# Performance work log

Hardware: AMD Instinct MI355X
Metric: run time of the kernel (lower is better)

The kernel has to match this reference:

```python
import jax, jax.numpy as jnp
import numpy as np
import math

HEADS = 8

def setup_inputs() -> dict:
    key = jax.random.key(0)
    k1, k2 = jax.random.split(key)
    B, C, H, W = 8, 512, 32, 32
    x = jax.random.normal(k1, (B, C, H, W), dtype=jnp.float32)
    # weight-norm 1x1 conv params: v ~ N(0, 0.05), g initialized to ||v|| (torch weight_norm default)
    proj_v = jax.random.normal(k2, (3 * C, C), dtype=jnp.float32) * 0.05
    proj_g = jnp.linalg.norm(proj_v, axis=1)
    proj_b = jnp.zeros((3 * C,), dtype=jnp.float32)
    return {"x": x, "proj_v": proj_v, "proj_g": proj_g, "proj_b": proj_b}

def reference(x, proj_v, proj_g, proj_b):
    B, C, H, W = x.shape
    heads = HEADS
    dim = C // heads
    N = H * W
    # weight-normalized 1x1 conv: w = g * v / ||v|| per output channel
    w = proj_g[:, None] * proj_v / jnp.linalg.norm(proj_v, axis=1, keepdims=True)
    c = jnp.einsum('oc,bchw->bohw', w, x) + proj_b[None, :, None, None]
    c = c.reshape(B, 3, heads, dim, N)
    q, k, v = c[:, 0], c[:, 1], c[:, 2]  # each (B, heads, dim, N)
    scale = 1.0 / math.sqrt(dim)
    attn = jnp.einsum('bhdq,bhdk->bhqk', q, k) * scale  # (B, heads, N, N)
    attn = jax.nn.softmax(attn, axis=-1)
    out = jnp.einsum('bhdk,bhqk->bhdq', v, attn)  # (B, heads, dim, N)
    return x + out.reshape(B, C, H, W)
```

## Files before the change

kernel.cpp:

```cpp
#include <hip/hip_runtime.h>

typedef _Float16 f16;
typedef _Float16 f16x2 __attribute__((ext_vector_type(2)));
typedef _Float16 f16x4 __attribute__((ext_vector_type(4)));
typedef _Float16 f16x8 __attribute__((ext_vector_type(8)));
typedef float f32x4 __attribute__((ext_vector_type(4)));
typedef unsigned int u32;

__device__ inline f32x4 mfma16(f16x8 a, f16x8 b, f32x4 c) {
    return __builtin_amdgcn_mfma_f32_16x16x32_f16(a, b, c, 0, 0, 0);
}

__device__ inline f16x2 pk2(float a, float b) {
    return __builtin_bit_cast(f16x2, __builtin_amdgcn_cvt_pkrtz(a, b));
}

__device__ inline void st8(f16* p, f16x8 v) {
    *(f16x4*)p = __builtin_shufflevector(v, v, 0, 1, 2, 3);
    *(f16x4*)(p + 4) = __builtin_shufflevector(v, v, 4, 5, 6, 7);
}
__device__ inline f16x8 ld8(const f16* p) {
    f16x4 lo = *(const f16x4*)p;
    f16x4 hi = *(const f16x4*)(p + 4);
    return __builtin_shufflevector(lo, hi, 0, 1, 2, 3, 4, 5, 6, 7);
}

__global__ __launch_bounds__(256) void prep_k(const float* __restrict__ pv,
                                              const float* __restrict__ pg,
                                              f16* __restrict__ w,
                                              const float* __restrict__ x,
                                              f16* __restrict__ xT) {
    int bid = blockIdx.x;
    if (bid < 1536) {
        int o = bid;
        const float* row = pv + (size_t)o * 512;
        float s = 0.f;
        for (int c = threadIdx.x; c < 512; c += 256) { float t = row[c]; s += t * t; }
        for (int off = 32; off; off >>= 1) s += __shfl_down(s, off, 64);
        __shared__ float red[4];
        int lane = threadIdx.x & 63, wid = threadIdx.x >> 6;
        if (lane == 0) red[wid] = s;
        __syncthreads();
        float tot = red[0] + red[1] + red[2] + red[3];
        float scale = pg[o] * rsqrtf(tot);
        for (int c = threadIdx.x; c < 512; c += 256)
            w[(size_t)o * 512 + c] = (f16)(row[c] * scale);
    } else {
        int t2 = bid - 1536;
        int n0 = (t2 & 31) * 32, c0 = ((t2 >> 5) & 15) * 32, b = t2 >> 9;
        int tx = threadIdx.x & 31, ty = threadIdx.x >> 5;
        __shared__ float t[32][33];
        const float* xb = x + (size_t)b * 512 * 1024;
        for (int i = 0; i < 4; i++)
            t[ty + 8 * i][tx] = xb[(size_t)(c0 + ty + 8 * i) * 1024 + n0 + tx];
        __syncthreads();
        f16* xTb = xT + (size_t)b * 1024 * 512;
        for (int i = 0; i < 4; i++)
            xTb[(size_t)(n0 + ty + 8 * i) * 512 + c0 + tx] = (f16)t[tx][ty + 8 * i];
    }
}

__global__ __launch_bounds__(256) void qkv_gemm_k(const f16* __restrict__ w,
                                                  const f16* __restrict__ xT,
                                                  const float* __restrict__ pb,
                                                  f16* __restrict__ qk,
                                                  f16* __restrict__ v) {
    __shared__ f16 lA[128 * 64];
    __shared__ f16 lB[128 * 64];
    int b = blockIdx.z;
    int oBase = blockIdx.y * 128;
    int nBase = blockIdx.x * 128;
    const f16* xb = xT + (size_t)b * 1024 * 512;
    int tid = threadIdx.x, lane = tid & 63, warp = tid >> 6;
    int wy = warp >> 1, wx = warp & 1;
    int quad = lane >> 4, l15 = lane & 15;

    int srow = lane >> 3;
    int phys = lane & 7;
    int schunk = phys ^ srow;
    const f16* aS[4]; const f16* bS[4]; int ldsOff[4];
    for (int j = 0; j < 4; j++) {
        int rb = (warp * 4 + j) * 8;
        aS[j] = w  + (size_t)(oBase + rb + srow) * 512 + schunk * 8;
        bS[j] = xb + (size_t)(nBase + rb + srow) * 512 + schunk * 8;
        ldsOff[j] = (rb + srow) * 64 + phys * 8;
    }
    int ph0 = (quad ^ (l15 & 7)) * 8;
    int ph1 = ((4 + quad) ^ (l15 & 7)) * 8;

    f16x8 rA[4], rB[4];
    for (int j = 0; j < 4; j++) {
        rA[j] = *(const f16x8*)aS[j];
        rB[j] = *(const f16x8*)bS[j];
    }

    f32x4 acc[4][4] = {};

    for (int i = 0; i < 8; i++) {
        __syncthreads();
        for (int j = 0; j < 4; j++) {
            *(f16x8*)&lA[ldsOff[j]] = rA[j];
            *(f16x8*)&lB[ldsOff[j]] = rB[j];
        }
        __syncthreads();
        if (i < 7) {
            int k0 = (i + 1) * 64;
            for (int j = 0; j < 4; j++) {
                rA[j] = *(const f16x8*)(aS[j] + k0);
                rB[j] = *(const f16x8*)(bS[j] + k0);
            }
        }
        for (int kh = 0; kh < 2; kh++) {
            int ph = kh ? ph1 : ph0;
            f16x8 af[4], bf[4];
            for (int mi = 0; mi < 4; mi++)
                af[mi] = *(f16x8*)&lA[(wy * 64 + mi * 16 + l15) * 64 + ph];
            for (int ni = 0; ni < 4; ni++)
                bf[ni] = *(f16x8*)&lB[(wx * 64 + ni * 16 + l15) * 64 + ph];
            for (int mi = 0; mi < 4; mi++)
                for (int ni = 0; ni < 4; ni++)
                    acc[mi][ni] = mfma16(af[mi], bf[ni], acc[mi][ni]);
        }
    }

    int selB = oBase >> 9;
    for (int mi = 0; mi < 4; mi++) {
        int oRow = oBase + wy * 64 + mi * 16 + quad * 4;
        int h = (oRow >> 6) & 7, d0 = oRow & 63;
        for (int ni = 0; ni < 4; ni++) {
            int n = nBase + wx * 64 + ni * 16 + l15;
            if (selB < 2) {
                float sc = selB == 0 ? 0.125f : 1.0f;
                f16x4 o4;
                o4[0] = (f16)((acc[mi][ni][0] + pb[oRow + 0]) * sc);
                o4[1] = (f16)((acc[mi][ni][1] + pb[oRow + 1]) * sc);
                o4[2] = (f16)((acc[mi][ni][2] + pb[oRow + 2]) * sc);
                o4[3] = (f16)((acc[mi][ni][3] + pb[oRow + 3]) * sc);
                *(f16x4*)&qk[((((size_t)b * 2 + selB) * 8 + h) * 1024 + n) * 64 + d0] = o4;
            } else {
                for (int reg = 0; reg < 4; reg++) {
                    float val = acc[mi][ni][reg] + pb[oRow + reg];
                    v[(((size_t)b * 8 + h) * 64 + d0 + reg) * 1024 + n] = (f16)val;
                }
            }
        }
    }
}

#define ALDK 68
__global__ __launch_bounds__(256) void attn_k(const f16* __restrict__ qk,
                                              const f16* __restrict__ vg,
                                              const float* __restrict__ x,
                                              float* __restrict__ out) {
    __shared__ __align__(16) f16 smem[(2 * 64 + 8 * 16) * ALDK];
    f16* lK = smem;
    f16* lV = smem + 64 * ALDK;
    f16* lPb = smem + 2 * 64 * ALDK;
    float* OT = (float*)smem;

    int bh = blockIdx.y;
    int b = bh >> 3, h = bh & 7;
    int qBase = blockIdx.x * 128;
    int tid = threadIdx.x, lane = tid & 63, warp = tid >> 6;
    int quad = lane >> 4, l15 = lane & 15;

    const f16* qbase = qk + (((size_t)b * 2 + 0) * 8 + h) * 1024 * 64;
    const f16* kbase = qk + (((size_t)b * 2 + 1) * 8 + h) * 1024 * 64;
    const f16* vbase = vg + ((size_t)b * 8 + h) * 64 * 1024;

    int q0 = qBase + warp * 32;
    f16x8 aq[2][2];
    for (int s = 0; s < 2; s++)
        for (int kh = 0; kh < 2; kh++)
            aq[s][kh] = *(const f16x8*)&qbase[(size_t)(q0 + s * 16 + l15) * 64 + kh * 32 + quad * 8];

    int sr0 = tid >> 3, sc0 = (tid & 7) * 8;
    int sr1 = (tid + 256) >> 3, sc1 = sc0;

    f16x8 rK[2], rV[2];
    rK[0] = *(const f16x8*)&kbase[(size_t)sr0 * 64 + sc0];
    rK[1] = *(const f16x8*)&kbase[(size_t)sr1 * 64 + sc1];
    rV[0] = *(const f16x8*)&vbase[(size_t)sr0 * 1024 + sc0];
    rV[1] = *(const f16x8*)&vbase[(size_t)sr1 * 1024 + sc1];

    f32x4 accO[2][4] = {};
    float l_cur[2] = {0.f, 0.f};

    for (int kt = 0; kt < 16; kt++) {
        __syncthreads();
        st8(&lK[sr0 * ALDK + sc0], rK[0]);
        st8(&lK[sr1 * ALDK + sc1], rK[1]);
        st8(&lV[sr0 * ALDK + sc0], rV[0]);
        st8(&lV[sr1 * ALDK + sc1], rV[1]);
        __syncthreads();
        if (kt < 15) {
            const f16* kb = kbase + (size_t)(kt + 1) * 64 * 64;
            rK[0] = *(const f16x8*)&kb[(size_t)sr0 * 64 + sc0];
            rK[1] = *(const f16x8*)&kb[(size_t)sr1 * 64 + sc1];
            rV[0] = *(const f16x8*)&vbase[(size_t)sr0 * 1024 + (kt + 1) * 64 + sc0];
            rV[1] = *(const f16x8*)&vbase[(size_t)sr1 * 1024 + (kt + 1) * 64 + sc1];
        }

        f32x4 st[2][4] = {};
        for (int mt = 0; mt < 4; mt++) {
            f16x8 ak0 = ld8(&lK[(mt * 16 + l15) * ALDK + 0 * 32 + quad * 8]);
            f16x8 ak1 = ld8(&lK[(mt * 16 + l15) * ALDK + 1 * 32 + quad * 8]);
            for (int s = 0; s < 2; s++) {
                st[s][mt] = mfma16(ak0, aq[s][0], st[s][mt]);
                st[s][mt] = mfma16(ak1, aq[s][1], st[s][mt]);
            }
        }

        for (int s = 0; s < 2; s++) {
            f16* lP = lPb + (warp * 2 + s) * 16 * ALDK;
            float rs0 = 0.f, rs1 = 0.f, rs2 = 0.f, rs3 = 0.f;
            for (int mt = 0; mt < 4; mt++) {
                float p0 = __expf(st[s][mt][0]);
                float p1 = __expf(st[s][mt][1]);
                float p2 = __expf(st[s][mt][2]);
                float p3 = __expf(st[s][mt][3]);
                rs0 += p0; rs1 += p1; rs2 += p2; rs3 += p3;
                f16x2 lo = pk2(p0, p1);
                f16x2 hi = pk2(p2, p3);
                f16x4 pk;
                pk[0] = lo[0]; pk[1] = lo[1]; pk[2] = hi[0]; pk[3] = hi[1];
                *(f16x4*)&lP[l15 * ALDK + mt * 16 + quad * 4] = pk;
            }
            float rs = (rs0 + rs1) + (rs2 + rs3);
            rs += __shfl_xor(rs, 16, 64);
            rs += __shfl_xor(rs, 32, 64);
            l_cur[s] += rs;
        }

        f16x8 bp[2][2];
        for (int s = 0; s < 2; s++) {
            f16* lP = lPb + (warp * 2 + s) * 16 * ALDK;
            bp[s][0] = ld8(&lP[l15 * ALDK + 0 * 32 + quad * 8]);
            bp[s][1] = ld8(&lP[l15 * ALDK + 1 * 32 + quad * 8]);
        }
        for (int dt = 0; dt < 4; dt++) {
            f16x8 av0 = ld8(&lV[(dt * 16 + l15) * ALDK + 0 * 32 + quad * 8]);
            f16x8 av1 = ld8(&lV[(dt * 16 + l15) * ALDK + 1 * 32 + quad * 8]);
            for (int s = 0; s < 2; s++) {
                accO[s][dt] = mfma16(av0, bp[s][0], accO[s][dt]);
                accO[s][dt] = mfma16(av1, bp[s][1], accO[s][dt]);
            }
        }
    }

    __syncthreads();
    for (int s = 0; s < 2; s++) {
        float rl = 1.0f / l_cur[s];
        for (int dt = 0; dt < 4; dt++)
            for (int r = 0; r < 4; r++)
                OT[(dt * 16 + quad * 4 + r) * 132 + warp * 32 + s * 16 + l15] =
                    accO[s][dt][r] * rl;
    }
    __syncthreads();
    for (int i = 0; i < 8; i++) {
        int cid = tid + 256 * i;
        int d = cid >> 5, qi = (cid & 31) * 4;
        float4 o4 = *(float4*)&OT[d * 132 + qi];
        size_t gi = ((size_t)b * 512 + h * 64 + d) * 1024 + qBase + qi;
        float4 xv = *(const float4*)&x[gi];
        o4.x += xv.x; o4.y += xv.y; o4.z += xv.z; o4.w += xv.w;
        *(float4*)&out[gi] = o4;
    }
}

extern "C" void kernel_launch(void* const* d_in, const int* in_sizes, int n_in,
                              void* d_out, int out_size, void* d_ws, size_t ws_size,
                              hipStream_t stream) {
    (void)in_sizes; (void)n_in; (void)out_size; (void)ws_size;
    const float* x  = (const float*)d_in[0];
    const float* pv = (const float*)d_in[1];
    const float* pg = (const float*)d_in[2];
    const float* pb = (const float*)d_in[3];
    float* out = (float*)d_out;

    char* ws = (char*)d_ws;
    f16* w   = (f16*)(ws);
    f16* xT  = (f16*)(ws + 1572864);
    f16* qk  = (f16*)(ws + 1572864 + 8388608);
    f16* v   = (f16*)(ws + 1572864 + 8388608 + 16777216);

    hipLaunchKernelGGL(prep_k,     dim3(5632),     dim3(256), 0, stream, pv, pg, w, x, xT);
    hipLaunchKernelGGL(qkv_gemm_k, dim3(8, 12, 8), dim3(256), 0, stream, w, xT, pb, qk, v);
    hipLaunchKernelGGL(attn_k,     dim3(8, 64),    dim3(256), 0, stream, qk, v, x, out);
}
```

Measured before the change: 137.3 us.

## Switch QKV GEMM and attention to 32x32x16 MFMA tiles

Both the QKV projection GEMM and the attention kernel now use the 32x32x16 f16 MFMA instruction instead of 16x16x32, with fragment loads, LDS swizzle offsets, the P staging layout and epilogue index mapping rewritten to match. Larger MFMA tiles reuse each operand fragment across more output elements, so fewer LDS reads and instructions are issued per FLOP. The row-sum reduction also needs one shuffle instead of two. The cost is larger accumulator vectors per lane, which raises register pressure, plus an LDS layout for P that could add bank conflicts.

```diff
diff --git a/kernel.cpp b/kernel.cpp
--- a/kernel.cpp
+++ b/kernel.cpp
@@ -5,10 +5,10 @@
 typedef _Float16 f16x4 __attribute__((ext_vector_type(4)));
 typedef _Float16 f16x8 __attribute__((ext_vector_type(8)));
 typedef float f32x4 __attribute__((ext_vector_type(4)));
-typedef unsigned int u32;
-
-__device__ inline f32x4 mfma16(f16x8 a, f16x8 b, f32x4 c) {
-    return __builtin_amdgcn_mfma_f32_16x16x32_f16(a, b, c, 0, 0, 0);
+typedef float f32x16 __attribute__((ext_vector_type(16)));
+
+__device__ inline f32x16 mfma32(f16x8 a, f16x8 b, f32x16 c) {
+    return __builtin_amdgcn_mfma_f32_32x32x16_f16(a, b, c, 0, 0, 0);
 }
 
 __device__ inline f16x2 pk2(float a, float b) {
@@ -73,7 +73,7 @@
     const f16* xb = xT + (size_t)b * 1024 * 512;
     int tid = threadIdx.x, lane = tid & 63, warp = tid >> 6;
     int wy = warp >> 1, wx = warp & 1;
-    int quad = lane >> 4, l15 = lane & 15;
+    int l31 = lane & 31, hi = lane >> 5;
 
     int srow = lane >> 3;
     int phys = lane & 7;
@@ -85,8 +85,9 @@
         bS[j] = xb + (size_t)(nBase + rb + srow) * 512 + schunk * 8;
         ldsOff[j] = (rb + srow) * 64 + phys * 8;
     }
-    int ph0 = (quad ^ (l15 & 7)) * 8;
-    int ph1 = ((4 + quad) ^ (l15 & 7)) * 8;
+    int phk[4];
+    for (int ks = 0; ks < 4; ks++)
+        phk[ks] = (((ks * 2 + hi) ^ (l31 & 7))) * 8;
 
     f16x8 rA[4], rB[4];
     for (int j = 0; j < 4; j++) {
@@ -94,7 +95,7 @@
         rB[j] = *(const f16x8*)bS[j];
     }
 
-    f32x4 acc[4][4] = {};
+    f32x16 acc[2][2] = {};
 
     for (int i = 0; i < 8; i++) {
         __syncthreads();
@@ -110,37 +111,36 @@
                 rB[j] = *(const f16x8*)(bS[j] + k0);
             }
         }
-        for (int kh = 0; kh < 2; kh++) {
-            int ph = kh ? ph1 : ph0;
-            f16x8 af[4], bf[4];
-            for (int mi = 0; mi < 4; mi++)
-                af[mi] = *(f16x8*)&lA[(wy * 64 + mi * 16 + l15) * 64 + ph];
-            for (int ni = 0; ni < 4; ni++)
-                bf[ni] = *(f16x8*)&lB[(wx * 64 + ni * 16 + l15) * 64 + ph];
-            for (int mi = 0; mi < 4; mi++)
-                for (int ni = 0; ni < 4; ni++)
-                    acc[mi][ni] = mfma16(af[mi], bf[ni], acc[mi][ni]);
+        for (int ks = 0; ks < 4; ks++) {
+            f16x8 af[2], bf[2];
+            for (int mi = 0; mi < 2; mi++)
+                af[mi] = *(f16x8*)&lA[(wy * 64 + mi * 32 + l31) * 64 + phk[ks]];
+            for (int ni = 0; ni < 2; ni++)
+                bf[ni] = *(f16x8*)&lB[(wx * 64 + ni * 32 + l31) * 64 + phk[ks]];
+            for (int mi = 0; mi < 2; mi++)
+                for (int ni = 0; ni < 2; ni++)
+                    acc[mi][ni] = mfma32(af[mi], bf[ni], acc[mi][ni]);
         }
     }
 
     int selB = oBase >> 9;
-    for (int mi = 0; mi < 4; mi++) {
-        int oRow = oBase + wy * 64 + mi * 16 + quad * 4;
-        int h = (oRow >> 6) & 7, d0 = oRow & 63;
-        for (int ni = 0; ni < 4; ni++) {
-            int n = nBase + wx * 64 + ni * 16 + l15;
-            if (selB < 2) {
-                float sc = selB == 0 ? 0.125f : 1.0f;
-                f16x4 o4;
-                o4[0] = (f16)((acc[mi][ni][0] + pb[oRow + 0]) * sc);
-                o4[1] = (f16)((acc[mi][ni][1] + pb[oRow + 1]) * sc);
-                o4[2] = (f16)((acc[mi][ni][2] + pb[oRow + 2]) * sc);
-                o4[3] = (f16)((acc[mi][ni][3] + pb[oRow + 3]) * sc);
-                *(f16x4*)&qk[((((size_t)b * 2 + selB) * 8 + h) * 1024 + n) * 64 + d0] = o4;
-            } else {
-                for (int reg = 0; reg < 4; reg++) {
-                    float val = acc[mi][ni][reg] + pb[oRow + reg];
-                    v[(((size_t)b * 8 + h) * 64 + d0 + reg) * 1024 + n] = (f16)val;
+    for (int mi = 0; mi < 2; mi++) {
+        for (int g = 0; g < 4; g++) {
+            int oR = oBase + wy * 64 + mi * 32 + 8 * g + 4 * hi;
+            int h = (oR >> 6) & 7, d0 = oR & 63;
+            for (int ni = 0; ni < 2; ni++) {
+                int n = nBase + wx * 64 + ni * 32 + l31;
+                if (selB < 2) {
+                    float sc = selB == 0 ? 0.125f : 1.0f;
+                    f16x4 o4;
+                    for (int r = 0; r < 4; r++)
+                        o4[r] = (f16)((acc[mi][ni][g * 4 + r] + pb[oR + r]) * sc);
+                    *(f16x4*)&qk[((((size_t)b * 2 + selB) * 8 + h) * 1024 + n) * 64 + d0] = o4;
+                } else {
+                    for (int r = 0; r < 4; r++) {
+                        float val = acc[mi][ni][g * 4 + r] + pb[oR + r];
+                        v[(((size_t)b * 8 + h) * 64 + d0 + r) * 1024 + n] = (f16)val;
+                    }
                 }
             }
         }
@@ -152,7 +152,7 @@
                                               const f16* __restrict__ vg,
                                               const float* __restrict__ x,
                                               float* __restrict__ out) {
-    __shared__ __align__(16) f16 smem[(2 * 64 + 8 * 16) * ALDK];
+    __shared__ __align__(16) f16 smem[(2 * 64 + 4 * 32) * ALDK];
     f16* lK = smem;
     f16* lV = smem + 64 * ALDK;
     f16* lPb = smem + 2 * 64 * ALDK;
@@ -162,17 +162,17 @@
     int b = bh >> 3, h = bh & 7;
     int qBase = blockIdx.x * 128;
     int tid = threadIdx.x, lane = tid & 63, warp = tid >> 6;
-    int quad = lane >> 4, l15 = lane & 15;
+    int l31 = lane & 31, hi = lane >> 5;
 
     const f16* qbase = qk + (((size_t)b * 2 + 0) * 8 + h) * 1024 * 64;
     const f16* kbase = qk + (((size_t)b * 2 + 1) * 8 + h) * 1024 * 64;
     const f16* vbase = vg + ((size_t)b * 8 + h) * 64 * 1024;
+    f16* lP = lPb + warp * 32 * ALDK;
 
     int q0 = qBase + warp * 32;
-    f16x8 aq[2][2];
-    for (int s = 0; s < 2; s++)
-        for (int kh = 0; kh < 2; kh++)
-            aq[s][kh] = *(const f16x8*)&qbase[(size_t)(q0 + s * 16 + l15) * 64 + kh * 32 + quad * 8];
+    f16x8 aq[4];
+    for (int ks = 0; ks < 4; ks++)
+        aq[ks] = *(const f16x8*)&qbase[(size_t)(q0 + l31) * 64 + ks * 16 + hi * 8];
 
     int sr0 = tid >> 3, sc0 = (tid & 7) * 8;
     int sr1 = (tid + 256) >> 3, sc1 = sc0;
@@ -183,8 +183,8 @@
     rV[0] = *(const f16x8*)&vbase[(size_t)sr0 * 1024 + sc0];
     rV[1] = *(const f16x8*)&vbase[(size_t)sr1 * 1024 + sc1];
 
-    f32x4 accO[2][4] = {};
-    float l_cur[2] = {0.f, 0.f};
+    f32x16 accO[2] = {};
+    float l_cur = 0.f;
 
     for (int kt = 0; kt < 16; kt++) {
         __syncthreads();
@@ -201,61 +201,45 @@
             rV[1] = *(const f16x8*)&vbase[(size_t)sr1 * 1024 + (kt + 1) * 64 + sc1];
         }
 
-        f32x4 st[2][4] = {};
-        for (int mt = 0; mt < 4; mt++) {
-            f16x8 ak0 = ld8(&lK[(mt * 16 + l15) * ALDK + 0 * 32 + quad * 8]);
-            f16x8 ak1 = ld8(&lK[(mt * 16 + l15) * ALDK + 1 * 32 + quad * 8]);
-            for (int s = 0; s < 2; s++) {
-                st[s][mt] = mfma16(ak0, aq[s][0], st[s][mt]);
-                st[s][mt] = mfma16(ak1, aq[s][1], st[s][mt]);
-            }
-        }
-
-        for (int s = 0; s < 2; s++) {
-            f16* lP = lPb + (warp * 2 + s) * 16 * ALDK;
-            float rs0 = 0.f, rs1 = 0.f, rs2 = 0.f, rs3 = 0.f;
-            for (int mt = 0; mt < 4; mt++) {
-                float p0 = __expf(st[s][mt][0]);
-                float p1 = __expf(st[s][mt][1]);
-                float p2 = __expf(st[s][mt][2]);
-                float p3 = __expf(st[s][mt][3]);
-                rs0 += p0; rs1 += p1; rs2 += p2; rs3 += p3;
+        f32x16 stt[2] = {};
+        for (int mt = 0; mt < 2; mt++)
+            for (int ks = 0; ks < 4; ks++) {
+                f16x8 ak = ld8(&lK[(mt * 32 + l31) * ALDK + ks * 16 + hi * 8]);
+                stt[mt] = mfma32(ak, aq[ks], stt[mt]);
+            }
+
+        float rs = 0.f;
+        for (int mt = 0; mt < 2; mt++)
+            for (int g = 0; g < 4; g++) {
+                float p0 = __expf(stt[mt][g * 4 + 0]);
+                float p1 = __expf(stt[mt][g * 4 + 1]);
+                float p2 = __expf(stt[mt][g * 4 + 2]);
+                float p3 = __expf(stt[mt][g * 4 + 3]);
+                rs += (p0 + p1) + (p2 + p3);
                 f16x2 lo = pk2(p0, p1);
-                f16x2 hi = pk2(p2, p3);
+                f16x2 hi2 = pk2(p2, p3);
                 f16x4 pk;
-                pk[0] = lo[0]; pk[1] = lo[1]; pk[2] = hi[0]; pk[3] = hi[1];
-                *(f16x4*)&lP[l15 * ALDK + mt * 16 + quad * 4] = pk;
-            }
-            float rs = (rs0 + rs1) + (rs2 + rs3);
-            rs += __shfl_xor(rs, 16, 64);
-            rs += __shfl_xor(rs, 32, 64);
-            l_cur[s] += rs;
-        }
-
-        f16x8 bp[2][2];
-        for (int s = 0; s < 2; s++) {
-            f16* lP = lPb + (warp * 2 + s) * 16 * ALDK;
-            bp[s][0] = ld8(&lP[l15 * ALDK + 0 * 32 + quad * 8]);
-            bp[s][1] = ld8(&lP[l15 * ALDK + 1 * 32 + quad * 8]);
-        }
-        for (int dt = 0; dt < 4; dt++) {
-            f16x8 av0 = ld8(&lV[(dt * 16 + l15) * ALDK + 0 * 32 + quad * 8]);
-            f16x8 av1 = ld8(&lV[(dt * 16 + l15) * ALDK + 1 * 32 + quad * 8]);
-            for (int s = 0; s < 2; s++) {
-                accO[s][dt] = mfma16(av0, bp[s][0], accO[s][dt]);
-                accO[s][dt] = mfma16(av1, bp[s][1], accO[s][dt]);
-            }
-        }
+                pk[0] = lo[0]; pk[1] = lo[1]; pk[2] = hi2[0]; pk[3] = hi2[1];
+                *(f16x4*)&lP[l31 * ALDK + mt * 32 + 8 * g + 4 * hi] = pk;
+            }
+        rs += __shfl_xor(rs, 32, 64);
+        l_cur += rs;
+
+        for (int dt = 0; dt < 2; dt++)
+            for (int ks = 0; ks < 4; ks++) {
+                f16x8 av = ld8(&lV[(dt * 32 + l31) * ALDK + ks * 16 + hi * 8]);
+                f16x8 bp = ld8(&lP[l31 * ALDK + ks * 16 + hi * 8]);
+                accO[dt] = mfma32(av, bp, accO[dt]);
+            }
     }
 
     __syncthreads();
-    for (int s = 0; s < 2; s++) {
-        float rl = 1.0f / l_cur[s];
-        for (int dt = 0; dt < 4; dt++)
+    float rl = 1.0f / l_cur;
+    for (int dt = 0; dt < 2; dt++)
+        for (int g = 0; g < 4; g++)
             for (int r = 0; r < 4; r++)
-                OT[(dt * 16 + quad * 4 + r) * 132 + warp * 32 + s * 16 + l15] =
-                    accO[s][dt][r] * rl;
-    }
+                OT[(dt * 32 + 8 * g + 4 * hi + r) * 132 + warp * 32 + l31] =
+                    accO[dt][g * 4 + r] * rl;
     __syncthreads();
     for (int i = 0; i < 8; i++) {
         int cid = tid + 256 * i;
```

After: 134.3 us. 1.02x faster.
